# Performance work log

Hardware: AMD Instinct MI355X
Metric: run time of the kernel (lower is better)

The kernel has to match this reference:

```python
import jax, jax.numpy as jnp
import numpy as np

B = 32        # decode batch (one new token per sequence)
S = 4096      # kv cache length per sequence
H = 32        # query heads
G = 2         # kv groups (multi-query groups)
D = 128       # head dim (kv_channels)
ROT = D // 2  # rotary dim = 64, is_neox_style=False (GPT-J interleaved)
HID = 4096    # hidden size
QKV = (H + 2 * G) * D  # 4608
BASE = 10000.0


def setup_inputs() -> dict:
    key = jax.random.key(0)
    ks = jax.random.split(key, 7)
    return {
        "hidden_states": jax.random.normal(ks[0], (B, HID), jnp.float32),
        "positions": jax.random.randint(ks[1], (B,), 0, S, jnp.int32),
        "k_cache": jax.random.normal(ks[2], (B, S, G, D), jnp.float32) * 0.5,
        "v_cache": jax.random.normal(ks[3], (B, S, G, D), jnp.float32) * 0.5,
        "W_qkv": jax.random.normal(ks[4], (HID, QKV), jnp.float32) * 0.02,
        "b_qkv": jax.random.normal(ks[5], (QKV,), jnp.float32) * 0.02,
        "W_dense": jax.random.normal(ks[6], (H * D, HID), jnp.float32) * 0.02,
    }


def _apply_rope(x, pos):
    # x: [b, n_heads, D]; GPT-J style interleaved rotation on first ROT dims
    inv_freq = 1.0 / (BASE ** (jnp.arange(0, ROT, 2, dtype=jnp.float32) / ROT))  # [ROT//2]
    freqs = pos[:, None].astype(jnp.float32) * inv_freq                          # [b, ROT//2]
    cos = jnp.cos(freqs)[:, None, :]
    sin = jnp.sin(freqs)[:, None, :]
    xr, xp = x[..., :ROT], x[..., ROT:]
    x1, x2 = xr[..., 0::2], xr[..., 1::2]
    o1 = x1 * cos - x2 * sin
    o2 = x2 * cos + x1 * sin
    rot = jnp.stack([o1, o2], axis=-1).reshape(x.shape[:-1] + (ROT,))
    return jnp.concatenate([rot, xp], axis=-1)


def reference(hidden_states, positions, k_cache, v_cache, W_qkv, b_qkv, W_dense):
    # fused QKV projection (MQA split: H query heads, G kv groups)
    qkv = hidden_states @ W_qkv + b_qkv                     # [B, QKV]
    q = qkv[:, : H * D].reshape(B, H, D)
    k = qkv[:, H * D : (H + G) * D].reshape(B, G, D)
    v = qkv[:, (H + G) * D :].reshape(B, G, D)

    # inline RoPE on q and new k
    q = _apply_rope(q, positions)
    k = _apply_rope(k, positions)

    # write new k/v into cache at the current position (paged-cache write)
    b_idx = jnp.arange(B)
    kc = k_cache.at[b_idx, positions].set(k)                # [B, S, G, D]
    vc = v_cache.at[b_idx, positions].set(v)

    # grouped-query attention over the cache, causal via context length
    scale = jnp.float32(D) ** -0.5
    qg = q.reshape(B, G, H // G, D)                         # map head h -> group h // (H/G)
    logits = jnp.einsum("bghd,bsgd->bghs", qg, kc) * scale  # [B, G, H/G, S]
    valid = jnp.arange(S)[None, :] <= positions[:, None]    # [B, S]
    logits = jnp.where(valid[:, None, None, :], logits, jnp.float32(-1e9))
    probs = jax.nn.softmax(logits, axis=-1)
    ctx = jnp.einsum("bghs,bsgd->bghd", probs, vc).reshape(B, H * D)

    return ctx @ W_dense                                    # [B, HID]
```

## Files before the change

kernel.cpp:

```cpp
#include <hip/hip_runtime.h>
#include <math.h>

#define Bz 32
#define Sz 4096
#define Hz 32
#define Gz 2
#define Dz 128
#define HIDz 4096
#define QKVz 4608
#define NCHc 32
#define KTs 16

static __device__ __forceinline__ void fma4(float4& a, float s, const float4& v) {
  a.x = fmaf(s, v.x, a.x);
  a.y = fmaf(s, v.y, a.y);
  a.z = fmaf(s, v.z, a.z);
  a.w = fmaf(s, v.w, a.w);
}
static __device__ __forceinline__ float dot4(const float4& a, const float4& b, float acc) {
  return fmaf(a.x, b.x, fmaf(a.y, b.y, fmaf(a.z, b.z, fmaf(a.w, b.w, acc))));
}
static __device__ __forceinline__ void gload16(const float* src, float* ldst) {
  __builtin_amdgcn_global_load_lds(
      (const __attribute__((address_space(1))) void*)src,
      (__attribute__((address_space(3))) void*)ldst, 16, 0, 0);
}

__global__ __launch_bounds__(256) void gemm_partial(
    const float* __restrict__ X, const float* __restrict__ W,
    float* __restrict__ part, int K, int N, int KH) {
  extern __shared__ float hl[];
  const int stride = KH + 4;
  const int t = threadIdx.x;
  const int k0 = blockIdx.y * KH;
  const int cols4 = KH >> 2;
  const int total4 = Bz * cols4;
  for (int fi = t; fi < total4; fi += 256) {
    const int row = fi / cols4;
    const int c4 = fi - row * cols4;
    const float4 v = *(const float4*)&X[(size_t)row * K + k0 + c4 * 4];
    *(float4*)&hl[row * stride + c4 * 4] = v;
  }
  __syncthreads();
  const int jl = t & 31;
  const int b0 = (t >> 5) * 4;
  const int j = blockIdx.x * 128 + jl * 4;
  float4 acc[4];
  #pragma unroll
  for (int i = 0; i < 4; i++) acc[i] = make_float4(0.f, 0.f, 0.f, 0.f);
  float4 wa[4], wb[4];
#define LDW(buf, kk)                                                      \
  { _Pragma("unroll") for (int r = 0; r < 4; ++r)                         \
      buf[r] = *(const float4*)&W[(size_t)(k0 + (kk) + r) * N + j]; }
#define FMAW(buf, kk)                                                     \
  { _Pragma("unroll") for (int bi = 0; bi < 4; ++bi) {                    \
      const float4 hb = *(const float4*)&hl[(b0 + bi) * stride + (kk)];   \
      fma4(acc[bi], hb.x, buf[0]);                                        \
      fma4(acc[bi], hb.y, buf[1]);                                        \
      fma4(acc[bi], hb.z, buf[2]);                                        \
      fma4(acc[bi], hb.w, buf[3]); } }
  LDW(wa, 0);
  for (int kk = 0; kk < KH; kk += 8) {
    LDW(wb, kk + 4);
    FMAW(wa, kk);
    if (kk + 8 < KH) LDW(wa, kk + 8);
    FMAW(wb, kk + 4);
  }
#undef LDW
#undef FMAW
  #pragma unroll
  for (int bi = 0; bi < 4; bi++) {
    *(float4*)&part[((size_t)blockIdx.y * Bz + b0 + bi) * N + j] = acc[bi];
  }
}

__global__ __launch_bounds__(256) void qkv_finish(
    const float* __restrict__ part, const float* __restrict__ bias,
    const int* __restrict__ positions, int KT,
    float* __restrict__ qrot, float* __restrict__ krot, float* __restrict__ vnew) {
  const int t = threadIdx.x;
  const int b = blockIdx.x;
  const int head = blockIdx.y * 4 + (t >> 6);
  const int tp = t & 63;
  const int j0 = head * Dz + tp * 2;
  float s0 = bias[j0];
  float s1 = bias[j0 + 1];
  for (int kt = 0; kt < KT; kt++) {
    const float2 p = *(const float2*)&part[((size_t)kt * Bz + b) * QKVz + j0];
    s0 += p.x;
    s1 += p.y;
  }
  float o0 = s0, o1 = s1;
  if (head < Hz + Gz && tp < 32) {
    const float invf = exp2f(-(float)tp * (13.287712379549449f / 32.0f));
    const float a = (float)positions[b] * invf;
    float sn, cs;
    sincosf(a, &sn, &cs);
    o0 = s0 * cs - s1 * sn;
    o1 = s1 * cs + s0 * sn;
  }
  if (head < Hz) {
    const float sc = 0.08838834764831845f;
    float2 o = make_float2(o0 * sc, o1 * sc);
    *(float2*)&qrot[((size_t)b * Hz + head) * Dz + tp * 2] = o;
  } else if (head < Hz + Gz) {
    float2 o = make_float2(o0, o1);
    *(float2*)&krot[((size_t)b * Gz + (head - Hz)) * Dz + tp * 2] = o;
  } else {
    float2 o = make_float2(s0, s1);
    *(float2*)&vnew[((size_t)b * Gz + (head - Hz - Gz)) * Dz + tp * 2] = o;
  }
}

__global__ __launch_bounds__(256, 2) void attn_unit(
    const float* __restrict__ qrot, const float* __restrict__ kcache,
    const float* __restrict__ vcache, const float* __restrict__ krot,
    const float* __restrict__ vnew, const int* __restrict__ positions,
    float* __restrict__ mbuf, float* __restrict__ lbuf, float* __restrict__ pacc) {
  __shared__ float qs[16 * 132];
  __shared__ float kbw[4][1024];
  __shared__ float plw[4][128];
  __shared__ float scw[4][16];
  __shared__ float ml[128];
  const int g = blockIdx.y, b = blockIdx.z, bx = blockIdx.x;
  const int pos = positions[b];
  const int lt = pos + 1;
  const int blo = (bx * lt) >> 5;
  const int bhi = ((bx + 1) * lt) >> 5;
  const int nr = bhi - blo;
  const int t = threadIdx.x, w = t >> 6, lane = t & 63;
  const int hq = lane >> 4, rq = (lane >> 3) & 1, cq = lane & 7;
  float* kw = kbw[w];
  float* plv = plw[w];

  for (int i = t; i < 512; i += 256) {
    const int h = i >> 5, c4 = i & 31;
    const float4 q = *(const float4*)&qrot[((size_t)b * Hz + g * 16 + h) * Dz + c4 * 4];
    *(float4*)&qs[h * 132 + c4 * 4] = q;
  }

  const float* krow_new = &krot[((size_t)b * Gz + g) * Dz];
  const float* vrow_new = &vnew[((size_t)b * Gz + g) * Dz];
  const size_t kvb = ((size_t)b * Sz) * (Gz * Dz) + (size_t)g * Dz;

#define STAGE(tile) {                                                              \
    const int sg_ = blo + (tile) * 32 + w * 8 + (lane >> 3);                       \
    const bool fr_ = (sg_ >= bhi) || (sg_ == pos);                                 \
    const float* kp_ = fr_ ? krow_new : &kcache[kvb + (size_t)sg_ * (Gz * Dz)];    \
    gload16(kp_ + (lane & 7) * 4,      &kw[0 * 256 + lane * 4]);                   \
    gload16(kp_ + (lane & 7) * 4 + 32, &kw[1 * 256 + lane * 4]);                   \
    gload16(kp_ + (lane & 7) * 4 + 64, &kw[2 * 256 + lane * 4]);                   \
    gload16(kp_ + (lane & 7) * 4 + 96, &kw[3 * 256 + lane * 4]); }

  float m_run[4], l_run[4];
  float2 A2[16];
  #pragma unroll
  for (int i = 0; i < 4; ++i) { m_run[i] = -1e30f; l_run[i] = 0.f; }
  #pragma unroll
  for (int h = 0; h < 16; ++h) A2[h] = make_float2(0.f, 0.f);

  const int ntw = (nr > w * 8) ? ((nr - w * 8 + 31) >> 5) : 0;
  __syncthreads();

  for (int tile = 0; tile < ntw; ++tile) {
    STAGE(tile);
    float lp[4][4];
    #pragma unroll
    for (int i = 0; i < 4; ++i)
      #pragma unroll
      for (int s = 0; s < 4; ++s) lp[i][s] = 0.f;
    #pragma unroll
    for (int j = 0; j < 4; ++j) {
      float4 kf[4];
      #pragma unroll
      for (int s = 0; s < 4; ++s)
        kf[s] = *(const float4*)&kw[j * 256 + ((rq * 4 + s) * 8 + cq) * 4];
      #pragma unroll
      for (int i = 0; i < 4; ++i) {
        const float4 qv = *(const float4*)&qs[(hq * 4 + i) * 132 + (cq + 8 * j) * 4];
        #pragma unroll
        for (int s = 0; s < 4; ++s) lp[i][s] = dot4(qv, kf[s], lp[i][s]);
      }
    }
    #pragma unroll
    for (int i = 0; i < 4; ++i)
      #pragma unroll
      for (int s = 0; s < 4; ++s) {
        lp[i][s] += __shfl_xor(lp[i][s], 1);
        lp[i][s] += __shfl_xor(lp[i][s], 2);
        lp[i][s] += __shfl_xor(lp[i][s], 4);
      }
    const int rbase = tile * 32 + w * 8 + rq * 4;
    #pragma unroll
    for (int s = 0; s < 4; ++s) {
      if (rbase + s >= nr) {
        #pragma unroll
        for (int i = 0; i < 4; ++i) lp[i][s] = -1e30f;
      }
    }
    float sc[4];
    #pragma unroll
    for (int i = 0; i < 4; ++i) {
      float tm = fmaxf(fmaxf(lp[i][0], lp[i][1]), fmaxf(lp[i][2], lp[i][3]));
      tm = fmaxf(tm, __shfl_xor(tm, 8));
      const float mn = fmaxf(m_run[i], tm);
      sc[i] = __expf(m_run[i] - mn);
      m_run[i] = mn;
      float ts = 0.f;
      #pragma unroll
      for (int s = 0; s < 4; ++s) {
        lp[i][s] = __expf(lp[i][s] - mn);
        ts += lp[i][s];
      }
      ts += __shfl_xor(ts, 8);
      l_run[i] = l_run[i] * sc[i] + ts;
    }
    if (cq == 0) {
      if (rq == 0) *(float4*)&scw[w][hq * 4] = make_float4(sc[0], sc[1], sc[2], sc[3]);
      #pragma unroll
      for (int s = 0; s < 4; ++s)
        *(float4*)&plv[(rq * 4 + s) * 16 + hq * 4] =
            make_float4(lp[0][s], lp[1][s], lp[2][s], lp[3][s]);
    }
    {
      const float4 s0 = *(const float4*)&scw[w][0];
      const float4 s1 = *(const float4*)&scw[w][4];
      const float4 s2 = *(const float4*)&scw[w][8];
      const float4 s3 = *(const float4*)&scw[w][12];
      A2[0].x *= s0.x;  A2[0].y *= s0.x;   A2[1].x *= s0.y;  A2[1].y *= s0.y;
      A2[2].x *= s0.z;  A2[2].y *= s0.z;   A2[3].x *= s0.w;  A2[3].y *= s0.w;
      A2[4].x *= s1.x;  A2[4].y *= s1.x;   A2[5].x *= s1.y;  A2[5].y *= s1.y;
      A2[6].x *= s1.z;  A2[6].y *= s1.z;   A2[7].x *= s1.w;  A2[7].y *= s1.w;
      A2[8].x *= s2.x;  A2[8].y *= s2.x;   A2[9].x *= s2.y;  A2[9].y *= s2.y;
      A2[10].x *= s2.z; A2[10].y *= s2.z;  A2[11].x *= s2.w; A2[11].y *= s2.w;
      A2[12].x *= s3.x; A2[12].y *= s3.x;  A2[13].x *= s3.y; A2[13].y *= s3.y;
      A2[14].x *= s3.z; A2[14].y *= s3.z;  A2[15].x *= s3.w; A2[15].y *= s3.w;
    }
    #pragma unroll
    for (int s = 0; s < 8; ++s) {
      const int sg = blo + tile * 32 + w * 8 + s;
      const float* vp = (sg >= bhi || sg == pos) ? vrow_new
                         : &vcache[kvb + (size_t)sg * (Gz * Dz)];
      const float2 v2 = *(const float2*)&vp[lane * 2];
      const float4 p0 = *(const float4*)&plv[s * 16 + 0];
      const float4 p1 = *(const float4*)&plv[s * 16 + 4];
      const float4 p2 = *(const float4*)&plv[s * 16 + 8];
      const float4 p3 = *(const float4*)&plv[s * 16 + 12];
      A2[0].x = fmaf(p0.x, v2.x, A2[0].x);   A2[0].y = fmaf(p0.x, v2.y, A2[0].y);
      A2[1].x = fmaf(p0.y, v2.x, A2[1].x);   A2[1].y = fmaf(p0.y, v2.y, A2[1].y);
      A2[2].x = fmaf(p0.z, v2.x, A2[2].x);   A2[2].y = fmaf(p0.z, v2.y, A2[2].y);
      A2[3].x = fmaf(p0.w, v2.x, A2[3].x);   A2[3].y = fmaf(p0.w, v2.y, A2[3].y);
      A2[4].x = fmaf(p1.x, v2.x, A2[4].x);   A2[4].y = fmaf(p1.x, v2.y, A2[4].y);
      A2[5].x = fmaf(p1.y, v2.x, A2[5].x);   A2[5].y = fmaf(p1.y, v2.y, A2[5].y);
      A2[6].x = fmaf(p1.z, v2.x, A2[6].x);   A2[6].y = fmaf(p1.z, v2.y, A2[6].y);
      A2[7].x = fmaf(p1.w, v2.x, A2[7].x);   A2[7].y = fmaf(p1.w, v2.y, A2[7].y);
      A2[8].x = fmaf(p2.x, v2.x, A2[8].x);   A2[8].y = fmaf(p2.x, v2.y, A2[8].y);
      A2[9].x = fmaf(p2.y, v2.x, A2[9].x);   A2[9].y = fmaf(p2.y, v2.y, A2[9].y);
      A2[10].x = fmaf(p2.z, v2.x, A2[10].x); A2[10].y = fmaf(p2.z, v2.y, A2[10].y);
      A2[11].x = fmaf(p2.w, v2.x, A2[11].x); A2[11].y = fmaf(p2.w, v2.y, A2[11].y);
      A2[12].x = fmaf(p3.x, v2.x, A2[12].x); A2[12].y = fmaf(p3.x, v2.y, A2[12].y);
      A2[13].x = fmaf(p3.y, v2.x, A2[13].x); A2[13].y = fmaf(p3.y, v2.y, A2[13].y);
      A2[14].x = fmaf(p3.z, v2.x, A2[14].x); A2[14].y = fmaf(p3.z, v2.y, A2[14].y);
      A2[15].x = fmaf(p3.w, v2.x, A2[15].x); A2[15].y = fmaf(p3.w, v2.y, A2[15].y);
    }
  }

  __syncthreads();
  if (cq == 0 && rq == 0) {
    *(float4*)&ml[w * 32 + hq * 4] = make_float4(m_run[0], m_run[1], m_run[2], m_run[3]);
    *(float4*)&ml[w * 32 + 16 + hq * 4] = make_float4(l_run[0], l_run[1], l_run[2], l_run[3]);
  }
  __syncthreads();
  float ew[16];
  #pragma unroll
  for (int h = 0; h < 16; ++h) {
    const float ms = fmaxf(fmaxf(ml[h], ml[32 + h]), fmaxf(ml[64 + h], ml[96 + h]));
    ew[h] = __expf(ml[w * 32 + h] - ms);
  }
  float* Aw = &kbw[0][0];
  for (int step = 0; step < 4; ++step) {
    if (w == step) {
      #pragma unroll
      for (int h = 0; h < 16; ++h) {
        float2 x;
        if (step == 0) {
          x = make_float2(ew[h] * A2[h].x, ew[h] * A2[h].y);
        } else {
          x = *(const float2*)&Aw[h * 132 + lane * 2];
          x.x = fmaf(ew[h], A2[h].x, x.x);
          x.y = fmaf(ew[h], A2[h].y, x.y);
        }
        *(float2*)&Aw[h * 132 + lane * 2] = x;
      }
    }
    __syncthreads();
  }
  const size_t cb = (size_t)(b * Gz + g) * NCHc + bx;
  for (int o = t; o < 512; o += 256) {
    const int hh = o >> 5, d4c = o & 31;
    *(float4*)&pacc[cb * 2048 + (size_t)hh * Dz + d4c * 4] =
        *(const float4*)&Aw[hh * 132 + d4c * 4];
  }
  if (t < 16) {
    const int hh = t;
    const float m0 = ml[hh], m1 = ml[32 + hh], m2 = ml[64 + hh], m3 = ml[96 + hh];
    const float msf = fmaxf(fmaxf(m0, m1), fmaxf(m2, m3));
    const float l = __expf(m0 - msf) * ml[16 + hh] + __expf(m1 - msf) * ml[48 + hh] +
                    __expf(m2 - msf) * ml[80 + hh] + __expf(m3 - msf) * ml[112 + hh];
    mbuf[cb * 16 + hh] = msf;
    lbuf[cb * 16 + hh] = l;
  }
#undef STAGE
}

__global__ __launch_bounds__(512) void attn_combine(
    const float* __restrict__ mbuf, const float* __restrict__ lbuf,
    const float* __restrict__ pacc, const int* __restrict__ positions,
    float* __restrict__ ctx) {
  const int bg = blockIdx.x;
  const int b = bg >> 1, g = bg & 1;
  const int t = threadIdx.x;
  const int h = t >> 5, dg = t & 31;
  const size_t mlb = (size_t)bg * NCHc * 16 + h;
  float mstar = -1e30f;
  for (int c = 0; c < NCHc; c++) mstar = fmaxf(mstar, mbuf[mlb + c * 16]);
  float lsum = 0.f;
  float4 A = make_float4(0.f, 0.f, 0.f, 0.f);
  for (int c = 0; c < NCHc; c++) {
    const float wv = __expf(mbuf[mlb + c * 16] - mstar);
    lsum += wv * lbuf[mlb + c * 16];
    const float4 p = *(const float4*)&pacc[((size_t)bg * NCHc + c) * 2048 + (size_t)h * Dz + dg * 4];
    fma4(A, wv, p);
  }
  const float inv = 1.0f / lsum;
  float4 o = make_float4(A.x * inv, A.y * inv, A.z * inv, A.w * inv);
  *(float4*)&ctx[(size_t)b * (Hz * Dz) + (g * 16 + h) * Dz + dg * 4] = o;
}

__global__ __launch_bounds__(256) void reduce_out(
    const float* __restrict__ part, float* __restrict__ out, int KT) {
  const int idx = blockIdx.x * 256 + threadIdx.x;
  const int b = idx >> 12;
  const int j = idx & 4095;
  float s = 0.f;
  for (int kt = 0; kt < KT; kt++) s += part[((size_t)kt * Bz + b) * HIDz + j];
  out[idx] = s;
}

extern "C" void kernel_launch(void* const* d_in, const int* in_sizes, int n_in,
                              void* d_out, int out_size, void* d_ws, size_t ws_size,
                              hipStream_t stream) {
  const float* hidden = (const float*)d_in[0];
  const int* positions = (const int*)d_in[1];
  const float* kcache = (const float*)d_in[2];
  const float* vcache = (const float*)d_in[3];
  const float* Wqkv = (const float*)d_in[4];
  const float* bqkv = (const float*)d_in[5];
  const float* Wd = (const float*)d_in[6];
  float* out = (float*)d_out;

  const int KT = KTs;
  const int KH = HIDz / KT;

  float* w = (float*)d_ws;
  float* p1 = w;    w += (size_t)KT * Bz * QKVz;
  float* qrot = w;  w += (size_t)Bz * Hz * Dz;
  float* krot = w;  w += (size_t)Bz * Gz * Dz;
  float* vnew = w;  w += (size_t)Bz * Gz * Dz;
  float* mbuf = w;  w += (size_t)Bz * Gz * NCHc * 16;
  float* lbuf = w;  w += (size_t)Bz * Gz * NCHc * 16;
  float* pacc = w;  w += (size_t)Bz * Gz * NCHc * 2048;
  float* ctx = w;

  const size_t smem = (size_t)Bz * (KH + 4) * sizeof(float);

  gemm_partial<<<dim3(QKVz / 128, KT), 256, smem, stream>>>(hidden, Wqkv, p1, HIDz, QKVz, KH);
  qkv_finish<<<dim3(Bz, 9), 256, 0, stream>>>(p1, bqkv, positions, KT, qrot, krot, vnew);
  attn_unit<<<dim3(NCHc, Gz, Bz), 256, 0, stream>>>(qrot, kcache, vcache, krot, vnew, positions,
                                                    mbuf, lbuf, pacc);
  attn_combine<<<dim3(Bz * Gz), 512, 0, stream>>>(mbuf, lbuf, pacc, positions, ctx);
  gemm_partial<<<dim3(HIDz / 128, KT), 256, smem, stream>>>(ctx, Wd, p1, Hz * Dz, HIDz, KH);
  reduce_out<<<dim3(Bz * HIDz / 256), 256, 0, stream>>>(p1, out, KT);
}
```

Before: 166.1 us.

## Split attention heads per block into halves to double grid and occupancy

```diff
diff --git a/kernel.cpp b/kernel.cpp
--- a/kernel.cpp
+++ b/kernel.cpp
@@ -112,17 +112,18 @@
   }
 }
 
-__global__ __launch_bounds__(256, 2) void attn_unit(
+__global__ __launch_bounds__(256, 4) void attn_unit(
     const float* __restrict__ qrot, const float* __restrict__ kcache,
     const float* __restrict__ vcache, const float* __restrict__ krot,
     const float* __restrict__ vnew, const int* __restrict__ positions,
     float* __restrict__ mbuf, float* __restrict__ lbuf, float* __restrict__ pacc) {
-  __shared__ float qs[16 * 132];
+  __shared__ float qs[8 * 132];
   __shared__ float kbw[4][1024];
-  __shared__ float plw[4][128];
-  __shared__ float scw[4][16];
+  __shared__ float plw[4][64];
+  __shared__ float scw[4][8];
   __shared__ float ml[128];
-  const int g = blockIdx.y, b = blockIdx.z, bx = blockIdx.x;
+  const int y = blockIdx.y, b = blockIdx.z, bx = blockIdx.x;
+  const int g = y >> 1;
   const int pos = positions[b];
   const int lt = pos + 1;
   const int blo = (bx * lt) >> 5;
@@ -133,9 +134,9 @@
   float* kw = kbw[w];
   float* plv = plw[w];
 
-  for (int i = t; i < 512; i += 256) {
-    const int h = i >> 5, c4 = i & 31;
-    const float4 q = *(const float4*)&qrot[((size_t)b * Hz + g * 16 + h) * Dz + c4 * 4];
+  {
+    const int h = t >> 5, c4 = t & 31;
+    const float4 q = *(const float4*)&qrot[((size_t)b * Hz + y * 8 + h) * Dz + c4 * 4];
     *(float4*)&qs[h * 132 + c4 * 4] = q;
   }
 
@@ -152,21 +153,21 @@
     gload16(kp_ + (lane & 7) * 4 + 64, &kw[2 * 256 + lane * 4]);                   \
     gload16(kp_ + (lane & 7) * 4 + 96, &kw[3 * 256 + lane * 4]); }
 
-  float m_run[4], l_run[4];
-  float2 A2[16];
-  #pragma unroll
-  for (int i = 0; i < 4; ++i) { m_run[i] = -1e30f; l_run[i] = 0.f; }
-  #pragma unroll
-  for (int h = 0; h < 16; ++h) A2[h] = make_float2(0.f, 0.f);
+  float m_run[2], l_run[2];
+  float2 A2[8];
+  #pragma unroll
+  for (int i = 0; i < 2; ++i) { m_run[i] = -1e30f; l_run[i] = 0.f; }
+  #pragma unroll
+  for (int h = 0; h < 8; ++h) A2[h] = make_float2(0.f, 0.f);
 
   const int ntw = (nr > w * 8) ? ((nr - w * 8 + 31) >> 5) : 0;
   __syncthreads();
 
   for (int tile = 0; tile < ntw; ++tile) {
     STAGE(tile);
-    float lp[4][4];
-    #pragma unroll
-    for (int i = 0; i < 4; ++i)
+    float lp[2][4];
+    #pragma unroll
+    for (int i = 0; i < 2; ++i)
       #pragma unroll
       for (int s = 0; s < 4; ++s) lp[i][s] = 0.f;
     #pragma unroll
@@ -176,14 +177,14 @@
       for (int s = 0; s < 4; ++s)
         kf[s] = *(const float4*)&kw[j * 256 + ((rq * 4 + s) * 8 + cq) * 4];
       #pragma unroll
-      for (int i = 0; i < 4; ++i) {
-        const float4 qv = *(const float4*)&qs[(hq * 4 + i) * 132 + (cq + 8 * j) * 4];
+      for (int i = 0; i < 2; ++i) {
+        const float4 qv = *(const float4*)&qs[(hq * 2 + i) * 132 + (cq + 8 * j) * 4];
         #pragma unroll
         for (int s = 0; s < 4; ++s) lp[i][s] = dot4(qv, kf[s], lp[i][s]);
       }
     }
     #pragma unroll
-    for (int i = 0; i < 4; ++i)
+    for (int i = 0; i < 2; ++i)
       #pragma unroll
       for (int s = 0; s < 4; ++s) {
         lp[i][s] += __shfl_xor(lp[i][s], 1);
@@ -194,13 +195,13 @@
     #pragma unroll
     for (int s = 0; s < 4; ++s) {
       if (rbase + s >= nr) {
-        #pragma unroll
-        for (int i = 0; i < 4; ++i) lp[i][s] = -1e30f;
-      }
-    }
-    float sc[4];
-    #pragma unroll
-    for (int i = 0; i < 4; ++i) {
+        lp[0][s] = -1e30f;
+        lp[1][s] = -1e30f;
+      }
+    }
+    float sc[2];
+    #pragma unroll
+    for (int i = 0; i < 2; ++i) {
       float tm = fmaxf(fmaxf(lp[i][0], lp[i][1]), fmaxf(lp[i][2], lp[i][3]));
       tm = fmaxf(tm, __shfl_xor(tm, 8));
       const float mn = fmaxf(m_run[i], tm);
@@ -216,25 +217,18 @@
       l_run[i] = l_run[i] * sc[i] + ts;
     }
     if (cq == 0) {
-      if (rq == 0) *(float4*)&scw[w][hq * 4] = make_float4(sc[0], sc[1], sc[2], sc[3]);
+      if (rq == 0) *(float2*)&scw[w][hq * 2] = make_float2(sc[0], sc[1]);
       #pragma unroll
       for (int s = 0; s < 4; ++s)
-        *(float4*)&plv[(rq * 4 + s) * 16 + hq * 4] =
-            make_float4(lp[0][s], lp[1][s], lp[2][s], lp[3][s]);
+        *(float2*)&plv[(rq * 4 + s) * 8 + hq * 2] = make_float2(lp[0][s], lp[1][s]);
     }
     {
       const float4 s0 = *(const float4*)&scw[w][0];
       const float4 s1 = *(const float4*)&scw[w][4];
-      const float4 s2 = *(const float4*)&scw[w][8];
-      const float4 s3 = *(const float4*)&scw[w][12];
-      A2[0].x *= s0.x;  A2[0].y *= s0.x;   A2[1].x *= s0.y;  A2[1].y *= s0.y;
-      A2[2].x *= s0.z;  A2[2].y *= s0.z;   A2[3].x *= s0.w;  A2[3].y *= s0.w;
-      A2[4].x *= s1.x;  A2[4].y *= s1.x;   A2[5].x *= s1.y;  A2[5].y *= s1.y;
-      A2[6].x *= s1.z;  A2[6].y *= s1.z;   A2[7].x *= s1.w;  A2[7].y *= s1.w;
-      A2[8].x *= s2.x;  A2[8].y *= s2.x;   A2[9].x *= s2.y;  A2[9].y *= s2.y;
-      A2[10].x *= s2.z; A2[10].y *= s2.z;  A2[11].x *= s2.w; A2[11].y *= s2.w;
-      A2[12].x *= s3.x; A2[12].y *= s3.x;  A2[13].x *= s3.y; A2[13].y *= s3.y;
-      A2[14].x *= s3.z; A2[14].y *= s3.z;  A2[15].x *= s3.w; A2[15].y *= s3.w;
+      A2[0].x *= s0.x; A2[0].y *= s0.x;  A2[1].x *= s0.y; A2[1].y *= s0.y;
+      A2[2].x *= s0.z; A2[2].y *= s0.z;  A2[3].x *= s0.w; A2[3].y *= s0.w;
+      A2[4].x *= s1.x; A2[4].y *= s1.x;  A2[5].x *= s1.y; A2[5].y *= s1.y;
+      A2[6].x *= s1.z; A2[6].y *= s1.z;  A2[7].x *= s1.w; A2[7].y *= s1.w;
     }
     #pragma unroll
     for (int s = 0; s < 8; ++s) {
@@ -242,46 +236,36 @@
       const float* vp = (sg >= bhi || sg == pos) ? vrow_new
                          : &vcache[kvb + (size_t)sg * (Gz * Dz)];
       const float2 v2 = *(const float2*)&vp[lane * 2];
-      const float4 p0 = *(const float4*)&plv[s * 16 + 0];
-      const float4 p1 = *(const float4*)&plv[s * 16 + 4];
-      const float4 p2 = *(const float4*)&plv[s * 16 + 8];
-      const float4 p3 = *(const float4*)&plv[s * 16 + 12];
-      A2[0].x = fmaf(p0.x, v2.x, A2[0].x);   A2[0].y = fmaf(p0.x, v2.y, A2[0].y);
-      A2[1].x = fmaf(p0.y, v2.x, A2[1].x);   A2[1].y = fmaf(p0.y, v2.y, A2[1].y);
-      A2[2].x = fmaf(p0.z, v2.x, A2[2].x);   A2[2].y = fmaf(p0.z, v2.y, A2[2].y);
-      A2[3].x = fmaf(p0.w, v2.x, A2[3].x);   A2[3].y = fmaf(p0.w, v2.y, A2[3].y);
-      A2[4].x = fmaf(p1.x, v2.x, A2[4].x);   A2[4].y = fmaf(p1.x, v2.y, A2[4].y);
-      A2[5].x = fmaf(p1.y, v2.x, A2[5].x);   A2[5].y = fmaf(p1.y, v2.y, A2[5].y);
-      A2[6].x = fmaf(p1.z, v2.x, A2[6].x);   A2[6].y = fmaf(p1.z, v2.y, A2[6].y);
-      A2[7].x = fmaf(p1.w, v2.x, A2[7].x);   A2[7].y = fmaf(p1.w, v2.y, A2[7].y);
-      A2[8].x = fmaf(p2.x, v2.x, A2[8].x);   A2[8].y = fmaf(p2.x, v2.y, A2[8].y);
-      A2[9].x = fmaf(p2.y, v2.x, A2[9].x);   A2[9].y = fmaf(p2.y, v2.y, A2[9].y);
-      A2[10].x = fmaf(p2.z, v2.x, A2[10].x); A2[10].y = fmaf(p2.z, v2.y, A2[10].y);
-      A2[11].x = fmaf(p2.w, v2.x, A2[11].x); A2[11].y = fmaf(p2.w, v2.y, A2[11].y);
-      A2[12].x = fmaf(p3.x, v2.x, A2[12].x); A2[12].y = fmaf(p3.x, v2.y, A2[12].y);
-      A2[13].x = fmaf(p3.y, v2.x, A2[13].x); A2[13].y = fmaf(p3.y, v2.y, A2[13].y);
-      A2[14].x = fmaf(p3.z, v2.x, A2[14].x); A2[14].y = fmaf(p3.z, v2.y, A2[14].y);
-      A2[15].x = fmaf(p3.w, v2.x, A2[15].x); A2[15].y = fmaf(p3.w, v2.y, A2[15].y);
+      const float4 p0 = *(const float4*)&plv[s * 8 + 0];
+      const float4 p1 = *(const float4*)&plv[s * 8 + 4];
+      A2[0].x = fmaf(p0.x, v2.x, A2[0].x);  A2[0].y = fmaf(p0.x, v2.y, A2[0].y);
+      A2[1].x = fmaf(p0.y, v2.x, A2[1].x);  A2[1].y = fmaf(p0.y, v2.y, A2[1].y);
+      A2[2].x = fmaf(p0.z, v2.x, A2[2].x);  A2[2].y = fmaf(p0.z, v2.y, A2[2].y);
+      A2[3].x = fmaf(p0.w, v2.x, A2[3].x);  A2[3].y = fmaf(p0.w, v2.y, A2[3].y);
+      A2[4].x = fmaf(p1.x, v2.x, A2[4].x);  A2[4].y = fmaf(p1.x, v2.y, A2[4].y);
+      A2[5].x = fmaf(p1.y, v2.x, A2[5].x);  A2[5].y = fmaf(p1.y, v2.y, A2[5].y);
+      A2[6].x = fmaf(p1.z, v2.x, A2[6].x);  A2[6].y = fmaf(p1.z, v2.y, A2[6].y);
+      A2[7].x = fmaf(p1.w, v2.x, A2[7].x);  A2[7].y = fmaf(p1.w, v2.y, A2[7].y);
     }
   }
 
   __syncthreads();
   if (cq == 0 && rq == 0) {
-    *(float4*)&ml[w * 32 + hq * 4] = make_float4(m_run[0], m_run[1], m_run[2], m_run[3]);
-    *(float4*)&ml[w * 32 + 16 + hq * 4] = make_float4(l_run[0], l_run[1], l_run[2], l_run[3]);
+    *(float2*)&ml[w * 16 + hq * 2] = make_float2(m_run[0], m_run[1]);
+    *(float2*)&ml[64 + w * 16 + hq * 2] = make_float2(l_run[0], l_run[1]);
   }
   __syncthreads();
-  float ew[16];
-  #pragma unroll
-  for (int h = 0; h < 16; ++h) {
-    const float ms = fmaxf(fmaxf(ml[h], ml[32 + h]), fmaxf(ml[64 + h], ml[96 + h]));
-    ew[h] = __expf(ml[w * 32 + h] - ms);
+  float ew[8];
+  #pragma unroll
+  for (int h = 0; h < 8; ++h) {
+    const float ms = fmaxf(fmaxf(ml[h], ml[16 + h]), fmaxf(ml[32 + h], ml[48 + h]));
+    ew[h] = __expf(ml[w * 16 + h] - ms);
   }
   float* Aw = &kbw[0][0];
   for (int step = 0; step < 4; ++step) {
     if (w == step) {
       #pragma unroll
-      for (int h = 0; h < 16; ++h) {
+      for (int h = 0; h < 8; ++h) {
         float2 x;
         if (step == 0) {
           x = make_float2(ew[h] * A2[h].x, ew[h] * A2[h].y);
@@ -295,20 +279,20 @@
     }
     __syncthreads();
   }
-  const size_t cb = (size_t)(b * Gz + g) * NCHc + bx;
-  for (int o = t; o < 512; o += 256) {
-    const int hh = o >> 5, d4c = o & 31;
-    *(float4*)&pacc[cb * 2048 + (size_t)hh * Dz + d4c * 4] =
+  const size_t cb = (size_t)(b * 4 + y) * NCHc + bx;
+  if (t < 256) {
+    const int hh = t >> 5, d4c = t & 31;
+    *(float4*)&pacc[cb * 1024 + (size_t)hh * Dz + d4c * 4] =
         *(const float4*)&Aw[hh * 132 + d4c * 4];
   }
-  if (t < 16) {
+  if (t < 8) {
     const int hh = t;
-    const float m0 = ml[hh], m1 = ml[32 + hh], m2 = ml[64 + hh], m3 = ml[96 + hh];
+    const float m0 = ml[hh], m1 = ml[16 + hh], m2 = ml[32 + hh], m3 = ml[48 + hh];
     const float msf = fmaxf(fmaxf(m0, m1), fmaxf(m2, m3));
-    const float l = __expf(m0 - msf) * ml[16 + hh] + __expf(m1 - msf) * ml[48 + hh] +
-                    __expf(m2 - msf) * ml[80 + hh] + __expf(m3 - msf) * ml[112 + hh];
-    mbuf[cb * 16 + hh] = msf;
-    lbuf[cb * 16 + hh] = l;
+    const float l = __expf(m0 - msf) * ml[64 + hh] + __expf(m1 - msf) * ml[80 + hh] +
+                    __expf(m2 - msf) * ml[96 + hh] + __expf(m3 - msf) * ml[112 + hh];
+    mbuf[cb * 8 + hh] = msf;
+    lbuf[cb * 8 + hh] = l;
   }
 #undef STAGE
 }
@@ -317,24 +301,25 @@
     const float* __restrict__ mbuf, const float* __restrict__ lbuf,
     const float* __restrict__ pacc, const int* __restrict__ positions,
     float* __restrict__ ctx) {
-  const int bg = blockIdx.x;
-  const int b = bg >> 1, g = bg & 1;
+  const int bgH = blockIdx.x;
+  const int b = bgH >> 2, y = bgH & 3;
   const int t = threadIdx.x;
-  const int h = t >> 5, dg = t & 31;
-  const size_t mlb = (size_t)bg * NCHc * 16 + h;
+  const int h = t >> 6, dg = t & 63;
   float mstar = -1e30f;
-  for (int c = 0; c < NCHc; c++) mstar = fmaxf(mstar, mbuf[mlb + c * 16]);
+  for (int c = 0; c < NCHc; c++) mstar = fmaxf(mstar, mbuf[((size_t)bgH * NCHc + c) * 8 + h]);
   float lsum = 0.f;
-  float4 A = make_float4(0.f, 0.f, 0.f, 0.f);
+  float2 A = make_float2(0.f, 0.f);
   for (int c = 0; c < NCHc; c++) {
-    const float wv = __expf(mbuf[mlb + c * 16] - mstar);
-    lsum += wv * lbuf[mlb + c * 16];
-    const float4 p = *(const float4*)&pacc[((size_t)bg * NCHc + c) * 2048 + (size_t)h * Dz + dg * 4];
-    fma4(A, wv, p);
+    const size_t cb = (size_t)bgH * NCHc + c;
+    const float wv = __expf(mbuf[cb * 8 + h] - mstar);
+    lsum += wv * lbuf[cb * 8 + h];
+    const float2 p = *(const float2*)&pacc[cb * 1024 + (size_t)h * Dz + dg * 2];
+    A.x = fmaf(wv, p.x, A.x);
+    A.y = fmaf(wv, p.y, A.y);
   }
   const float inv = 1.0f / lsum;
-  float4 o = make_float4(A.x * inv, A.y * inv, A.z * inv, A.w * inv);
-  *(float4*)&ctx[(size_t)b * (Hz * Dz) + (g * 16 + h) * Dz + dg * 4] = o;
+  float2 o = make_float2(A.x * inv, A.y * inv);
+  *(float2*)&ctx[(size_t)b * (Hz * Dz) + (y * 8 + h) * Dz + dg * 2] = o;
 }
 
 __global__ __launch_bounds__(256) void reduce_out(
@@ -367,18 +352,18 @@
   float* qrot = w;  w += (size_t)Bz * Hz * Dz;
   float* krot = w;  w += (size_t)Bz * Gz * Dz;
   float* vnew = w;  w += (size_t)Bz * Gz * Dz;
-  float* mbuf = w;  w += (size_t)Bz * Gz * NCHc * 16;
-  float* lbuf = w;  w += (size_t)Bz * Gz * NCHc * 16;
-  float* pacc = w;  w += (size_t)Bz * Gz * NCHc * 2048;
+  float* mbuf = w;  w += (size_t)Bz * 4 * NCHc * 8;
+  float* lbuf = w;  w += (size_t)Bz * 4 * NCHc * 8;
+  float* pacc = w;  w += (size_t)Bz * 4 * NCHc * 1024;
   float* ctx = w;
 
   const size_t smem = (size_t)Bz * (KH + 4) * sizeof(float);
 
   gemm_partial<<<dim3(QKVz / 128, KT), 256, smem, stream>>>(hidden, Wqkv, p1, HIDz, QKVz, KH);
   qkv_finish<<<dim3(Bz, 9), 256, 0, stream>>>(p1, bqkv, positions, KT, qrot, krot, vnew);
-  attn_unit<<<dim3(NCHc, Gz, Bz), 256, 0, stream>>>(qrot, kcache, vcache, krot, vnew, positions,
-                                                    mbuf, lbuf, pacc);
-  attn_combine<<<dim3(Bz * Gz), 512, 0, stream>>>(mbuf, lbuf, pacc, positions, ctx);
+  attn_unit<<<dim3(NCHc, 4, Bz), 256, 0, stream>>>(qrot, kcache, vcache, krot, vnew, positions,
+                                                   mbuf, lbuf, pacc);
+  attn_combine<<<dim3(Bz * 4), 512, 0, stream>>>(mbuf, lbuf, pacc, positions, ctx);
   gemm_partial<<<dim3(HIDz / 128, KT), 256, smem, stream>>>(ctx, Wd, p1, Hz * Dz, HIDz, KH);
   reduce_out<<<dim3(Bz * HIDz / 256), 256, 0, stream>>>(p1, out, KT);
 }
```

Result: slower. 214.0 us (+28.9%).
